# Kernel tuning notes

Measured on AMD Instinct MI355X. Metric: run time of the kernel, lower is better.

The kernel has to match this reference:

```python
import jax, jax.numpy as jnp
import numpy as np
import math

B, S, D, H, FF = 2, 2048, 1024, 16, 4096
HD = D // H
EPS = 1e-5


def setup_inputs() -> dict:
    key = jax.random.key(0)
    ks = jax.random.split(key, 16)
    w = lambda k, shape: (jax.random.normal(k, shape, jnp.float32) * 0.02)
    future = jnp.triu(jnp.ones((S, S), dtype=bool), k=1)
    causal_mask = jnp.where(future, -jnp.inf, 0.0).astype(jnp.float32)
    return {
        "src": jax.random.normal(ks[0], (B, S, D), jnp.float32),
        "causal_mask": causal_mask,
        "Wq": w(ks[1], (D, D)), "bq": jnp.zeros((D,), jnp.float32),
        "Wk": w(ks[2], (D, D)), "bk": jnp.zeros((D,), jnp.float32),
        "Wv": w(ks[3], (D, D)), "bv": jnp.zeros((D,), jnp.float32),
        "Wo": w(ks[4], (D, D)), "bo": jnp.zeros((D,), jnp.float32),
        "W1": w(ks[5], (D, FF)), "b1": jnp.zeros((FF,), jnp.float32),
        "W2": w(ks[6], (FF, D)), "b2": jnp.zeros((D,), jnp.float32),
        "ln1_g": jnp.ones((D,), jnp.float32), "ln1_b": jnp.zeros((D,), jnp.float32),
        "ln2_g": jnp.ones((D,), jnp.float32), "ln2_b": jnp.zeros((D,), jnp.float32),
    }


def _layernorm(x, g, b):
    mu = jnp.mean(x, axis=-1, keepdims=True)
    var = jnp.mean((x - mu) ** 2, axis=-1, keepdims=True)
    return (x - mu) * jax.lax.rsqrt(var + EPS) * g + b


def reference(src, causal_mask, Wq, bq, Wk, bk, Wv, bv, Wo, bo,
              W1, b1, W2, b2, ln1_g, ln1_b, ln2_g, ln2_b):
    # QKV projections, split heads: [B,S,D] -> [B,H,S,HD]
    def split_heads(x):
        return x.reshape(B, S, H, HD).transpose(0, 2, 1, 3)

    q = split_heads(src @ Wq + bq)
    k = split_heads(src @ Wk + bk)
    v = split_heads(src @ Wv + bv)

    # scores: [B,H,S,S]; attn_mask = causal_mask broadcast over batch, then head dim
    scores = jnp.einsum("bhqd,bhkd->bhqk", q, k) / math.sqrt(HD)
    scores = scores + causal_mask[None, None, :, :]
    # scores[scores != scores] = 0
    scores = jnp.where(jnp.isnan(scores), 0.0, scores)
    # rows that are entirely inf -> 0
    mask_all_inf = jnp.all(jnp.isinf(scores), axis=-1, keepdims=True)
    scores = jnp.where(mask_all_inf, 0.0, scores)
    attn = jax.nn.softmax(scores, axis=-1)
    attn = jnp.where(jnp.isnan(attn), 0.0, attn)

    ctx = jnp.einsum("bhqk,bhkd->bhqd", attn, v)
    ctx = ctx.transpose(0, 2, 1, 3).reshape(B, S, D)
    attn_out = ctx @ Wo + bo

    x = _layernorm(src + attn_out, ln1_g, ln1_b)
    ff = jax.nn.relu(x @ W1 + b1) @ W2 + b2
    return _layernorm(x + ff, ln2_g, ln2_b)
```

## Files before the change

kernel.cpp:

```cpp
#include <hip/hip_runtime.h>

#define SS 2048
#define DD 1024
#define HH 16
#define HDIM 64
#define BB 2
#define FFD 4096
#define MR (BB*SS)
#define QKVLD 3072

typedef __bf16 bf16;
typedef __bf16 bf16x4 __attribute__((ext_vector_type(4)));
typedef __bf16 bf16x8 __attribute__((ext_vector_type(8)));
typedef float f32x4 __attribute__((ext_vector_type(4)));

struct P4 { bf16* p[4]; };
struct TP4 { const float* src[4]; bf16* dst[4]; };

__device__ inline f32x4 mfma32(bf16x8 a, bf16x8 b, f32x4 c) {
  return __builtin_amdgcn_mfma_f32_16x16x32_bf16(a, b, c, 0, 0, 0);
}

__device__ inline void gload_lds16(const void* g, void* l) {
  __builtin_amdgcn_global_load_lds(
      (const __attribute__((address_space(1))) void*)g,
      (__attribute__((address_space(3))) void*)l, 16, 0, 0);
}

#if defined(__has_builtin)
#if __has_builtin(__builtin_amdgcn_exp2f)
#define HAVE_EXP2_BUILTIN 1
#endif
#endif
__device__ inline float fast_exp2(float x) {
#ifdef HAVE_EXP2_BUILTIN
  return __builtin_amdgcn_exp2f(x);
#else
  float r; asm("v_exp_f32 %0, %1" : "=v"(r) : "v"(x)); return r;
#endif
}

__global__ __launch_bounds__(256)
void cvt_bf16_kernel(const float* __restrict__ in, bf16* __restrict__ out, int n) {
  int i = (blockIdx.x * 256 + threadIdx.x) * 4;
  if (i >= n) return;
  float4 v = *(const float4*)(in + i);
  bf16x4 o;
  o[0] = (bf16)v.x; o[1] = (bf16)v.y; o[2] = (bf16)v.z; o[3] = (bf16)v.w;
  *(bf16x4*)(out + i) = o;
}

__global__ __launch_bounds__(256)
void concat_bias_kernel(const float* __restrict__ bq, const float* __restrict__ bk,
                        const float* __restrict__ bv, float* __restrict__ out) {
  int i = blockIdx.x * 256 + threadIdx.x;
  out[i] = i < 1024 ? bq[i] : (i < 2048 ? bk[i - 1024] : bv[i - 2048]);
}

__global__ __launch_bounds__(256)
void transpose_w4_kernel(TP4 t) {
  __shared__ float tl[32][33];
  const float* W = t.src[blockIdx.z];
  bf16* Wt = t.dst[blockIdx.z];
  int tx = threadIdx.x & 31, ty = threadIdx.x >> 5;
  int n0 = blockIdx.x * 32, k0 = blockIdx.y * 32;
  #pragma unroll
  for (int i = 0; i < 4; ++i)
    tl[ty + i*8][tx] = W[(size_t)(k0 + ty + i*8) * DD + n0 + tx];
  __syncthreads();
  #pragma unroll
  for (int i = 0; i < 4; ++i)
    Wt[(size_t)(n0 + ty + i*8) * DD + k0 + tx] = (bf16)tl[tx][ty + i*8];
}

__global__ __launch_bounds__(256)
void transpose_w_kernel(const float* __restrict__ W, bf16* __restrict__ Wt,
                        int K, int N) {
  __shared__ float t[32][33];
  int tx = threadIdx.x & 31, ty = threadIdx.x >> 5;
  int n0 = blockIdx.x * 32, k0 = blockIdx.y * 32;
  #pragma unroll
  for (int i = 0; i < 4; ++i)
    t[ty + i*8][tx] = W[(size_t)(k0 + ty + i*8) * N + n0 + tx];
  __syncthreads();
  #pragma unroll
  for (int i = 0; i < 4; ++i)
    Wt[(size_t)(n0 + ty + i*8) * K + k0 + tx] = (bf16)t[tx][ty + i*8];
}

__global__ __launch_bounds__(256)
void transpose_v_kernel(const bf16* __restrict__ V2d, bf16* __restrict__ Vt) {
  __shared__ bf16 t[32][33];
  int tx = threadIdx.x & 31, ty = threadIdx.x >> 5;
  int s0 = blockIdx.x * 32, d0 = blockIdx.y * 32;
  int bh = blockIdx.z;
  int b = bh >> 4, h = bh & 15;
  #pragma unroll
  for (int i = 0; i < 4; ++i)
    t[ty + i*8][tx] = V2d[(size_t)(b*SS + s0 + ty + i*8) * QKVLD + h*HDIM + d0 + tx];
  __syncthreads();
  #pragma unroll
  for (int i = 0; i < 4; ++i)
    Vt[((size_t)bh*HDIM + d0 + ty + i*8) * SS + s0 + tx] = t[tx][ty + i*8];
}

template<int OUT_BF16, int RELU, int SPLITK>
__global__ __launch_bounds__(512)
void gemm256(const bf16* __restrict__ A, const bf16* __restrict__ Bt,
             const float* __restrict__ bias, void* __restrict__ Cout,
             P4 part, int Ndim, int Kdim) {
  __shared__ bf16 Asm[3][256 * 64];
  __shared__ bf16 Bsm[2][256 * 64];
  const int gx = gridDim.x, gy = gridDim.y;
  const int gxy = gx * gy;
  const int nwg = gxy * gridDim.z;
  const int lin = (blockIdx.z * gy + blockIdx.y) * gx + blockIdx.x;
  const int swz = (lin & 7) * (nwg >> 3) + (lin >> 3);
  int bz = 0, rem = swz;
  if (SPLITK > 1) { bz = swz / gxy; rem = swz - bz * gxy; }
  const int by = rem / gx, bx = rem - by * gx;
  const int m0 = by * 256, n0 = bx * 256;
  const int tid = threadIdx.x;
  const int wave = tid >> 6, lane = tid & 63;
  const int g = lane >> 4, r = lane & 15;
  const int wr = wave >> 2, wn = wave & 3;
  const int kstart = bz * (Kdim / SPLITK);

  const int srow = wave * 8 + (lane >> 3);
  const int skslot = (lane & 7) ^ (lane >> 3);
  const bf16* Ag = A + (size_t)(m0 + srow) * Kdim + kstart + skslot * 8;
  const bf16* Bg = Bt + (size_t)(n0 + srow) * Kdim + kstart + skslot * 8;

  f32x4 acc[8][4] = {};
  const int NT = (Kdim / SPLITK) >> 6;

  auto stageA = [&](int t) {
    if (t >= NT) return;
    const int kb = t << 6;
    bf16* Ad = Asm[t % 3];
    #pragma unroll
    for (int j = 0; j < 4; ++j)
      gload_lds16(Ag + (size_t)j * 64 * Kdim + kb, Ad + (j * 64 + wave * 8) * 64);
  };
  auto stageB = [&](int t) {
    if (t >= NT) return;
    const int kb = t << 6;
    bf16* Bd = Bsm[t & 1];
    #pragma unroll
    for (int j = 0; j < 4; ++j)
      gload_lds16(Bg + (size_t)j * 64 * Kdim + kb, Bd + (j * 64 + wave * 8) * 64);
  };

  stageA(0);
  stageB(0);
  stageA(1);
  asm volatile("s_waitcnt vmcnt(4)" ::: "memory");
  asm volatile("s_barrier" ::: "memory");

  for (int t = 0; t < NT; ++t) {
    const bf16* Ab = Asm[t % 3];
    const bf16* Bb = Bsm[t & 1];
    bf16x8 bfr[4][2];
    #pragma unroll
    for (int i = 0; i < 4; ++i) {
      const int rowb = wn * 64 + i * 16 + r;
      #pragma unroll
      for (int kk = 0; kk < 2; ++kk)
        bfr[i][kk] = *(const bf16x8*)(Bb + rowb * 64 + (((kk * 4 + g) ^ (r & 7)) * 8));
    }
    #pragma unroll
    for (int ph = 0; ph < 2; ++ph) {
      bf16x8 af[4][2];
      #pragma unroll
      for (int i = 0; i < 4; ++i) {
        const int row = wr * 128 + (ph * 4 + i) * 16 + r;
        #pragma unroll
        for (int kk = 0; kk < 2; ++kk)
          af[i][kk] = *(const bf16x8*)(Ab + row * 64 + (((kk * 4 + g) ^ (r & 7)) * 8));
      }
      if (ph == 0) stageB(t + 1);
      if (ph == 1) stageA(t + 2);
      asm volatile("s_barrier" ::: "memory");
      __builtin_amdgcn_s_setprio(1);
      #pragma unroll
      for (int i = 0; i < 4; ++i)
        #pragma unroll
        for (int jn = 0; jn < 4; ++jn)
          #pragma unroll
          for (int kk = 0; kk < 2; ++kk)
            acc[ph * 4 + i][jn] = mfma32(af[i][kk], bfr[jn][kk], acc[ph * 4 + i][jn]);
      __builtin_amdgcn_s_setprio(0);
      asm volatile("s_barrier" ::: "memory");
    }
    if (t + 1 < NT) {
      if (t + 2 < NT) asm volatile("s_waitcnt vmcnt(4)" ::: "memory");
      else            asm volatile("s_waitcnt vmcnt(0)" ::: "memory");
      asm volatile("s_barrier" ::: "memory");
    }
  }

  #pragma unroll
  for (int mi = 0; mi < 8; ++mi) {
    #pragma unroll
    for (int ni = 0; ni < 4; ++ni) {
      const int col = n0 + wn * 64 + ni * 16 + r;
      const float bv = (SPLITK > 1) ? 0.f : bias[col];
      #pragma unroll
      for (int jj = 0; jj < 4; ++jj) {
        const int row = m0 + wr * 128 + mi * 16 + g * 4 + jj;
        float v = acc[mi][ni][jj] + bv;
        if (RELU) v = fmaxf(v, 0.f);
        if (SPLITK > 1) part.p[bz][(size_t)row * Ndim + col] = (bf16)v;
        else if (OUT_BF16) ((bf16*)Cout)[(size_t)row * Ndim + col] = (bf16)v;
        else               ((float*)Cout)[(size_t)row * Ndim + col] = v;
      }
    }
  }
}

__global__ __launch_bounds__(256)
void attn_kernel(const bf16* __restrict__ Q2d, const bf16* __restrict__ K2d,
                 const bf16* __restrict__ Vt, bf16* __restrict__ ctx) {
  __shared__ bf16 Ks[2 * 4096];
  __shared__ bf16 Vs[2 * 4096];
  const int tid = threadIdx.x;
  const int wave = tid >> 6;
  const int lane = tid & 63;
  const int g = lane >> 4, r = lane & 15;
  const int lin = blockIdx.y * gridDim.x + blockIdx.x;
  const int swz = (lin & 7) * 64 + (lin >> 3);
  const int p = swz & 15;
  const int bh = swz >> 4;
  const int b = bh >> 4, h = bh & 15;

  const int strow = wave * 16 + (lane >> 2);
  const int lslot = (lane & 3) ^ ((lane >> 3) & 3);
  const bf16* srcK0 = K2d + (size_t)(b*SS + strow) * QKVLD + h*HDIM + lslot * 8;
  const bf16* srcK1 = srcK0 + 32;
  const bf16* srcV0 = Vt + ((size_t)bh*HDIM + strow) * SS + lslot * 8;
  const bf16* srcV1 = srcV0 + 32;

  auto sw = [](int row, int s) { return row * 32 + ((s ^ ((row >> 1) & 3)) * 8); };

  const int kr0 = 8 * (r >> 2) + (r & 3);
  const int oKa0 = sw(kr0,      g), oKb0 = 2048 + oKa0;
  const int oKa1 = sw(kr0 +  4, g), oKb1 = 2048 + oKa1;
  const int oKa2 = sw(kr0 + 32, g), oKb2 = 2048 + oKa2;
  const int oKa3 = sw(kr0 + 36, g), oKb3 = 2048 + oKa3;
  int oV[4];
  #pragma unroll
  for (int c = 0; c < 4; ++c) oV[c] = sw(c * 16 + r, g);

  const float K2 = 0.18033688f;
  bf16x8 onesf;
  #pragma unroll
  for (int j = 0; j < 8; ++j) onesf[j] = (bf16)1.0f;

  #pragma unroll
  for (int tt = 0; tt < 2; ++tt) {
    const int tile = tt ? (31 - p) : p;
    const int q0 = tile * 64 + wave * 16;
    const int qg = q0 + r;
    const bf16* qp = Q2d + (size_t)(b*SS + q0 + r) * QKVLD + h * HDIM;
    const bf16x8 qf0 = *(const bf16x8*)(qp + g * 8);
    const bf16x8 qf1 = *(const bf16x8*)(qp + 32 + g * 8);
    f32x4 ov[4] = {};
    f32x4 lacc = {};
    const int nst = tile + 1;
    {
      bf16* kb = Ks + wave * 512;
      bf16* vb = Vs + wave * 512;
      gload_lds16(srcK0, kb);
      gload_lds16(srcK1, kb + 2048);
      gload_lds16(srcV0, vb);
      gload_lds16(srcV1, vb + 2048);
    }
    __syncthreads();
    int cur = 0;
    for (int st = 0; st < nst; ++st) {
      const int k0 = st * 64;
      if (st + 1 < nst) {
        const int kn = k0 + 64;
        bf16* kb = Ks + (cur ^ 1) * 4096 + wave * 512;
        bf16* vb = Vs + (cur ^ 1) * 4096 + wave * 512;
        gload_lds16(srcK0 + (size_t)kn * QKVLD, kb);
        gload_lds16(srcK1 + (size_t)kn * QKVLD, kb + 2048);
        gload_lds16(srcV0 + kn, vb);
        gload_lds16(srcV1 + kn, vb + 2048);
      }
      const bf16* Kb = Ks + cur * 4096;
      const bf16* Vb = Vs + cur * 4096;
      f32x4 c0 = {}, c1 = {}, c2 = {}, c3 = {};
      __builtin_amdgcn_s_setprio(1);
      c0 = mfma32(*(const bf16x8*)(Kb + oKa0), qf0, c0);
      c1 = mfma32(*(const bf16x8*)(Kb + oKa1), qf0, c1);
      c2 = mfma32(*(const bf16x8*)(Kb + oKa2), qf0, c2);
      c3 = mfma32(*(const bf16x8*)(Kb + oKa3), qf0, c3);
      c0 = mfma32(*(const bf16x8*)(Kb + oKb0), qf1, c0);
      c1 = mfma32(*(const bf16x8*)(Kb + oKb1), qf1, c1);
      c2 = mfma32(*(const bf16x8*)(Kb + oKb2), qf1, c2);
      c3 = mfma32(*(const bf16x8*)(Kb + oKb3), qf1, c3);
      __builtin_amdgcn_s_setprio(0);
      float p0[4], p1[4], p2[4], p3[4];
      const bool need_mask = (k0 + 63 > qg);
      #pragma unroll
      for (int j = 0; j < 4; ++j) {
        float s0 = c0[j] * K2;
        float s1 = c1[j] * K2;
        float s2 = c2[j] * K2;
        float s3 = c3[j] * K2;
        if (need_mask) {
          if (k0 + 8*g + j > qg)          s0 = -3.0e38f;
          if (k0 + 8*g + 4 + j > qg)      s1 = -3.0e38f;
          if (k0 + 32 + 8*g + j > qg)     s2 = -3.0e38f;
          if (k0 + 32 + 8*g + 4 + j > qg) s3 = -3.0e38f;
        }
        p0[j] = fast_exp2(s0);
        p1[j] = fast_exp2(s1);
        p2[j] = fast_exp2(s2);
        p3[j] = fast_exp2(s3);
      }
      bf16x8 pfa, pfb;
      #pragma unroll
      for (int j = 0; j < 4; ++j) {
        pfa[j] = (bf16)p0[j]; pfa[4 + j] = (bf16)p1[j];
        pfb[j] = (bf16)p2[j]; pfb[4 + j] = (bf16)p3[j];
      }
      __builtin_amdgcn_s_setprio(1);
      #pragma unroll
      for (int c = 0; c < 4; ++c) {
        bf16x8 vfa = *(const bf16x8*)(Vb + oV[c]);
        bf16x8 vfb = *(const bf16x8*)(Vb + 2048 + oV[c]);
        ov[c] = mfma32(pfa, vfa, ov[c]);
        ov[c] = mfma32(pfb, vfb, ov[c]);
      }
      lacc = mfma32(pfa, onesf, lacc);
      lacc = mfma32(pfb, onesf, lacc);
      __builtin_amdgcn_s_setprio(0);
      __syncthreads();
      cur ^= 1;
    }
    #pragma unroll
    for (int j = 0; j < 4; ++j) {
      const float inv = 1.f / lacc[j];
      const int row = b*SS + q0 + 4*g + j;
      #pragma unroll
      for (int c = 0; c < 4; ++c)
        ctx[(size_t)row * DD + h*HDIM + c*16 + r] = (bf16)(ov[c][j] * inv);
    }
  }
}

template<int WRITEB>
__global__ __launch_bounds__(256)
void ln_bf4_kernel(const float* __restrict__ a, P4 part, const float* __restrict__ cb,
                   const float* __restrict__ gam, const float* __restrict__ bet,
                   float* __restrict__ outf, bf16* __restrict__ outb) {
  const int row = blockIdx.x;
  const int tid = threadIdx.x;
  const size_t base = (size_t)row * DD + tid * 4;
  float4 va = *(const float4*)(a + base);
  bf16x4 u0 = *(const bf16x4*)(part.p[0] + base);
  bf16x4 u1 = *(const bf16x4*)(part.p[1] + base);
  bf16x4 u2 = *(const bf16x4*)(part.p[2] + base);
  bf16x4 u3 = *(const bf16x4*)(part.p[3] + base);
  float4 vb4 = *(const float4*)(cb + tid * 4);
  float x0 = va.x + ((float)u0[0] + (float)u1[0]) + ((float)u2[0] + (float)u3[0]) + vb4.x;
  float x1 = va.y + ((float)u0[1] + (float)u1[1]) + ((float)u2[1] + (float)u3[1]) + vb4.y;
  float x2 = va.z + ((float)u0[2] + (float)u1[2]) + ((float)u2[2] + (float)u3[2]) + vb4.z;
  float x3 = va.w + ((float)u0[3] + (float)u1[3]) + ((float)u2[3] + (float)u3[3]) + vb4.w;
  float s  = x0 + x1 + x2 + x3;
  float s2 = x0*x0 + x1*x1 + x2*x2 + x3*x3;
  #pragma unroll
  for (int off = 32; off > 0; off >>= 1) {
    s  += __shfl_xor(s,  off);
    s2 += __shfl_xor(s2, off);
  }
  __shared__ float red[8];
  const int wv = tid >> 6;
  if ((tid & 63) == 0) { red[wv] = s; red[wv + 4] = s2; }
  __syncthreads();
  s  = red[0] + red[1] + red[2] + red[3];
  s2 = red[4] + red[5] + red[6] + red[7];
  const float mu  = s * (1.f / DD);
  const float var = s2 * (1.f / DD) - mu * mu;
  const float rs  = rsqrtf(var + 1e-5f);
  float4 vg = *(const float4*)(gam + tid * 4);
  float4 vb = *(const float4*)(bet + tid * 4);
  float y0 = (x0 - mu) * rs * vg.x + vb.x;
  float y1 = (x1 - mu) * rs * vg.y + vb.y;
  float y2 = (x2 - mu) * rs * vg.z + vb.z;
  float y3 = (x3 - mu) * rs * vg.w + vb.w;
  float4 yo; yo.x = y0; yo.y = y1; yo.z = y2; yo.w = y3;
  *(float4*)(outf + base) = yo;
  if (WRITEB) {
    bf16x4 ob;
    ob[0] = (bf16)y0; ob[1] = (bf16)y1; ob[2] = (bf16)y2; ob[3] = (bf16)y3;
    *(bf16x4*)(outb + base) = ob;
  }
}

extern "C" void kernel_launch(void* const* d_in, const int* in_sizes, int n_in,
                              void* d_out, int out_size, void* d_ws, size_t ws_size,
                              hipStream_t stream) {
  const float* src  = (const float*)d_in[0];
  const float* Wq   = (const float*)d_in[2];
  const float* bq   = (const float*)d_in[3];
  const float* Wk   = (const float*)d_in[4];
  const float* bk   = (const float*)d_in[5];
  const float* Wv   = (const float*)d_in[6];
  const float* bv   = (const float*)d_in[7];
  const float* Wo   = (const float*)d_in[8];
  const float* bo   = (const float*)d_in[9];
  const float* W1   = (const float*)d_in[10];
  const float* b1   = (const float*)d_in[11];
  const float* W2   = (const float*)d_in[12];
  const float* b2   = (const float*)d_in[13];
  const float* ln1g = (const float*)d_in[14];
  const float* ln1b = (const float*)d_in[15];
  const float* ln2g = (const float*)d_in[16];
  const float* ln2b = (const float*)d_in[17];

  char* ws = (char*)d_ws;
  const size_t MB = 1024 * 1024;
  bf16* wqkvt = (bf16*)(ws + 0 * MB);
  bf16* wot   = (bf16*)(ws + 6 * MB);
  bf16* w1t   = (bf16*)(ws + 8 * MB);
  bf16* w2t   = (bf16*)(ws + 16 * MB);
  bf16* bsrc  = (bf16*)(ws + 24 * MB);
  bf16* xb    = bsrc;
  bf16* qkv   = (bf16*)(ws + 32 * MB);
  bf16* vt    = (bf16*)(ws + 56 * MB);
  bf16* ctx   = (bf16*)(ws + 64 * MB);
  bf16* ff1   = qkv;
  float* xf   = (float*)(ws + 72 * MB);
  float* bqkv = (float*)(ws + 88 * MB);
  float* outp = (float*)d_out;

  P4 wop;
  wop.p[0] = (bf16*)(ws + 32 * MB);
  wop.p[1] = (bf16*)(ws + 40 * MB);
  wop.p[2] = (bf16*)(ws + 48 * MB);
  wop.p[3] = (bf16*)(ws + 56 * MB);
  P4 fp;
  fp.p[0] = (bf16*)(ws + 0 * MB);
  fp.p[1] = (bf16*)(ws + 8 * MB);
  fp.p[2] = (bf16*)(ws + 24 * MB);
  fp.p[3] = (bf16*)(ws + 64 * MB);

  cvt_bf16_kernel<<<(MR * DD) / 1024, 256, 0, stream>>>(src, bsrc, MR * DD);
  TP4 tp;
  tp.src[0] = Wq; tp.dst[0] = wqkvt;
  tp.src[1] = Wk; tp.dst[1] = wqkvt + 1024*1024;
  tp.src[2] = Wv; tp.dst[2] = wqkvt + 2048*1024;
  tp.src[3] = Wo; tp.dst[3] = wot;
  transpose_w4_kernel<<<dim3(32, 32, 4), 256, 0, stream>>>(tp);
  transpose_w_kernel<<<dim3(128, 32), 256, 0, stream>>>(W1, w1t, DD, FFD);
  transpose_w_kernel<<<dim3(32, 128), 256, 0, stream>>>(W2, w2t, FFD, DD);
  concat_bias_kernel<<<12, 256, 0, stream>>>(bq, bk, bv, bqkv);

  gemm256<1, 0, 1><<<dim3(QKVLD / 256, MR / 256), 512, 0, stream>>>(bsrc, wqkvt, bqkv, qkv, P4{}, QKVLD, DD);
  transpose_v_kernel<<<dim3(SS / 32, HDIM / 32, BB * HH), 256, 0, stream>>>(qkv + 2048, vt);

  attn_kernel<<<dim3(16, BB * HH), 256, 0, stream>>>(qkv, qkv + 1024, vt, ctx);

  gemm256<0, 0, 4><<<dim3(DD / 256, MR / 256, 4), 512, 0, stream>>>(ctx, wot, nullptr, nullptr, wop, DD, DD);
  ln_bf4_kernel<1><<<MR, 256, 0, stream>>>(src, wop, bo, ln1g, ln1b, xf, xb);

  gemm256<1, 1, 1><<<dim3(FFD / 256, MR / 256), 512, 0, stream>>>(xb, w1t, b1, ff1, P4{}, FFD, DD);
  gemm256<0, 0, 4><<<dim3(DD / 256, MR / 256, 4), 512, 0, stream>>>(ff1, w2t, nullptr, nullptr, fp, DD, FFD);
  ln_bf4_kernel<0><<<MR, 256, 0, stream>>>(xf, fp, b2, ln2g, ln2b, outp, nullptr);
}
```

Before: 219.7 us.

## Load GEMM A operand directly from global into registers, bypassing LDS

```diff
diff --git a/kernel.cpp b/kernel.cpp
--- a/kernel.cpp
+++ b/kernel.cpp
@@ -109,7 +109,6 @@
 void gemm256(const bf16* __restrict__ A, const bf16* __restrict__ Bt,
              const float* __restrict__ bias, void* __restrict__ Cout,
              P4 part, int Ndim, int Kdim) {
-  __shared__ bf16 Asm[3][256 * 64];
   __shared__ bf16 Bsm[2][256 * 64];
   const int gx = gridDim.x, gy = gridDim.y;
   const int gxy = gx * gy;
@@ -128,20 +127,12 @@
 
   const int srow = wave * 8 + (lane >> 3);
   const int skslot = (lane & 7) ^ (lane >> 3);
-  const bf16* Ag = A + (size_t)(m0 + srow) * Kdim + kstart + skslot * 8;
   const bf16* Bg = Bt + (size_t)(n0 + srow) * Kdim + kstart + skslot * 8;
+  const bf16* Agl = A + (size_t)(m0 + wr * 128 + r) * Kdim + kstart + g * 8;
 
   f32x4 acc[8][4] = {};
   const int NT = (Kdim / SPLITK) >> 6;
 
-  auto stageA = [&](int t) {
-    if (t >= NT) return;
-    const int kb = t << 6;
-    bf16* Ad = Asm[t % 3];
-    #pragma unroll
-    for (int j = 0; j < 4; ++j)
-      gload_lds16(Ag + (size_t)j * 64 * Kdim + kb, Ad + (j * 64 + wave * 8) * 64);
-  };
   auto stageB = [&](int t) {
     if (t >= NT) return;
     const int kb = t << 6;
@@ -151,15 +142,23 @@
       gload_lds16(Bg + (size_t)j * 64 * Kdim + kb, Bd + (j * 64 + wave * 8) * 64);
   };
 
-  stageA(0);
   stageB(0);
-  stageA(1);
-  asm volatile("s_waitcnt vmcnt(4)" ::: "memory");
+  asm volatile("s_waitcnt vmcnt(0)" ::: "memory");
   asm volatile("s_barrier" ::: "memory");
 
   for (int t = 0; t < NT; ++t) {
-    const bf16* Ab = Asm[t % 3];
     const bf16* Bb = Bsm[t & 1];
+    stageB(t + 1);
+    __builtin_amdgcn_sched_barrier(0);
+    bf16x8 af[8][2];
+    {
+      const bf16* ap = Agl + (t << 6);
+      #pragma unroll
+      for (int i = 0; i < 8; ++i)
+        #pragma unroll
+        for (int kk = 0; kk < 2; ++kk)
+          af[i][kk] = *(const bf16x8*)(ap + (size_t)(i * 16) * Kdim + kk * 32);
+    }
     bf16x8 bfr[4][2];
     #pragma unroll
     for (int i = 0; i < 4; ++i) {
@@ -168,35 +167,17 @@
       for (int kk = 0; kk < 2; ++kk)
         bfr[i][kk] = *(const bf16x8*)(Bb + rowb * 64 + (((kk * 4 + g) ^ (r & 7)) * 8));
     }
+    __builtin_amdgcn_s_setprio(1);
     #pragma unroll
-    for (int ph = 0; ph < 2; ++ph) {
-      bf16x8 af[4][2];
-      #pragma unroll
-      for (int i = 0; i < 4; ++i) {
-        const int row = wr * 128 + (ph * 4 + i) * 16 + r;
+    for (int i = 0; i < 8; ++i)
+      #pragma unroll
+      for (int jn = 0; jn < 4; ++jn)
         #pragma unroll
         for (int kk = 0; kk < 2; ++kk)
-          af[i][kk] = *(const bf16x8*)(Ab + row * 64 + (((kk * 4 + g) ^ (r & 7)) * 8));
-      }
-      if (ph == 0) stageB(t + 1);
-      if (ph == 1) stageA(t + 2);
+          acc[i][jn] = mfma32(af[i][kk], bfr[jn][kk], acc[i][jn]);
+    __builtin_amdgcn_s_setprio(0);
+    if (t + 1 < NT)
       asm volatile("s_barrier" ::: "memory");
-      __builtin_amdgcn_s_setprio(1);
-      #pragma unroll
-      for (int i = 0; i < 4; ++i)
-        #pragma unroll
-        for (int jn = 0; jn < 4; ++jn)
-          #pragma unroll
-          for (int kk = 0; kk < 2; ++kk)
-            acc[ph * 4 + i][jn] = mfma32(af[i][kk], bfr[jn][kk], acc[ph * 4 + i][jn]);
-      __builtin_amdgcn_s_setprio(0);
-      asm volatile("s_barrier" ::: "memory");
-    }
-    if (t + 1 < NT) {
-      if (t + 2 < NT) asm volatile("s_waitcnt vmcnt(4)" ::: "memory");
-      else            asm volatile("s_waitcnt vmcnt(0)" ::: "memory");
-      asm volatile("s_barrier" ::: "memory");
-    }
   }
 
   #pragma unroll
```

Result: slower. 368.3 us (+67.7%).
